# Kernel tuning notes

Measured on AMD Instinct MI355X. Metric: run time of the kernel, lower is better.

## Reference

```python
import jax, jax.numpy as jnp
import numpy as np

VOCAB = 40000
EMB = 128
INNER = 128
Q_LEN = 20


def setup_inputs() -> dict:
    key = jax.random.key(0)
    ks = jax.random.split(key, 16)
    B, S, NB = 32, 512, 20
    std = 0.1
    inp = {
        "memories": jax.random.normal(ks[0], (B, S, NB, EMB), jnp.float32),
        "stories": jax.random.normal(ks[1], (B, S, EMB), jnp.float32),
        "stories_mask": jnp.ones((B, S), jnp.float32),
        "queries": jax.random.randint(ks[2], (B, Q_LEN), 0, VOCAB, jnp.int32),
        "keys": jax.random.randint(ks[3], (NB,), 0, VOCAB, jnp.int32),
        # learned parameters
        "emb_table": jax.random.normal(ks[4], (VOCAB, EMB), jnp.float32) * std,
        "mult_mask": jnp.ones((Q_LEN, EMB), jnp.float32),
        "A": jax.random.normal(ks[5], (EMB, INNER), jnp.float32) * std,
        "Bm": jax.random.normal(ks[6], (EMB, INNER), jnp.float32) * std,
        "C": jax.random.normal(ks[7], (EMB, INNER), jnp.float32) * std,
        "v": jnp.ones((INNER,), jnp.float32),
        "D": jax.random.normal(ks[8], (EMB, INNER), jnp.float32) * std,
        "E": jax.random.normal(ks[9], (EMB, INNER), jnp.float32) * std,
        "F": jax.random.normal(ks[10], (EMB, INNER), jnp.float32) * std,
        "w": jnp.ones((INNER,), jnp.float32),
        "H": jax.random.normal(ks[11], (EMB, EMB), jnp.float32) * std,
        "R": jax.random.normal(ks[12], (EMB, VOCAB), jnp.float32) * std,
    }
    return inp


def reference(memories, stories, stories_mask, queries, keys,
              emb_table, mult_mask, A, Bm, C, v, D, E, F, w, H, R):
    # _reduce_query: embed tokens, apply positional multiplicative mask, sum over positions
    u = jnp.sum(emb_table[queries] * mult_mask, axis=1)            # [B, emb]

    # intratemporal (Bahdanau-style) attention over memory blocks
    ia = jnp.einsum('bsne,ei->bsni', memories, A)                  # [B,S,NB,inner]
    kb = emb_table[keys] @ Bm                                      # [NB,inner]
    qc = u @ C                                                     # [B,inner]
    intr_align = jnp.sum(v * jnp.tanh(ia + kb[None, None] + qc[:, None, None]), axis=3)  # [B,S,NB]
    intr_attn = jax.nn.softmax(intr_align, axis=2)[..., None]      # [B,S,NB,1]
    temporal_memory = jnp.sum(intr_attn * memories, axis=2)        # [B,S,emb]

    # temporal attention over story sentences (with sentence term E, softmax activation)
    td = temporal_memory @ D                                       # [B,S,inner]
    te = stories @ E                                               # [B,S,inner]
    tf = (u @ F)[:, None]                                          # [B,1,inner]
    temporal_align_unmasked = jnp.sum(w * jnp.tanh(td + te + tf), axis=2)  # [B,S]
    temporal_align = temporal_align_unmasked * stories_mask
    # softmax branch: additive -inf mask where stories_mask == 0 (inf*0 NaNs zeroed in torch)
    masked_logits = jnp.where(stories_mask != 0, temporal_align, -jnp.inf)
    temporal_attn = jax.nn.softmax(masked_logits, axis=1)          # [B,S]

    # output readout (standard memory-network head)
    o = jnp.sum(temporal_attn[..., None] * temporal_memory, axis=1)  # [B,emb]
    logits = (o + u @ H) @ R                                         # [B,vocab]
    return logits
```

## Files before the change

### kernel.cpp

```cpp
#include <hip/hip_runtime.h>
#include <hip/hip_bf16.h>

#define B_   32
#define S_   512
#define NB_  20
#define EMB_ 128
#define VOC_ 40000

typedef float f32x4 __attribute__((ext_vector_type(4)));
typedef _Float16 f16x8 __attribute__((ext_vector_type(8)));
typedef __fp16 fp16x2 __attribute__((ext_vector_type(2)));

union FragH { uint4 u; f16x8 h; };
union H2 { fp16x2 h; unsigned u; };

__device__ __forceinline__ unsigned pk2(float a, float b){
  H2 t; t.h = __builtin_amdgcn_cvt_pkrtz(a, b);
  return t.u;
}
__device__ __forceinline__ unsigned short f2h(float x){
  _Float16 h = (_Float16)x;
  return __builtin_bit_cast(unsigned short, h);
}
__device__ __forceinline__ float tanh_fast(float x){
  float xx = fminf(fmaxf(x, -15.f), 15.f);
  float e2 = __builtin_amdgcn_exp2f(xx * 2.8853900817779268f);
  float r  = __builtin_amdgcn_rcpf(e2 + 1.f);
  return fmaf(-2.f, r, 1.f);
}


__global__ __launch_bounds__(128) void prep_kernel(
    const int* __restrict__ queries, const int* __restrict__ keys,
    const float* __restrict__ emb, const float* __restrict__ mmask,
    const float* __restrict__ A, const float* __restrict__ Bm,
    const float* __restrict__ C, const float* __restrict__ D,
    const float* __restrict__ E, const float* __restrict__ F,
    const float* __restrict__ H,
    float* __restrict__ qc_w, float* __restrict__ tf_w,
    float* __restrict__ uh_w, float* __restrict__ kb_w,
    unsigned short* __restrict__ afrag, unsigned short* __restrict__ w2frag)
{
  int bid = blockIdx.x, tid = threadIdx.x;
  if (bid < 32) {
    __shared__ float ulds[128];
    int b = bid;
    float s = 0.f;
    for (int q=0;q<NB_;q++){
      int tok = queries[b*NB_+q];
      s += emb[tok*128+tid]*mmask[q*128+tid];
    }
    ulds[tid] = s;
    __syncthreads();
    float sq=0.f, sf=0.f, sh=0.f;
    for (int e=0;e<128;e++){
      float uv = ulds[e];
      sq += uv*C[e*128+tid];
      sf += uv*F[e*128+tid];
      sh += uv*H[e*128+tid];
    }
    qc_w[b*128+tid]=sq; tf_w[b*128+tid]=sf; uh_w[b*128+tid]=sh;
  } else if (bid < 52) {
    __shared__ float ek[128];
    int n = bid-32;
    int tok = keys[n];
    ek[tid] = emb[tok*128+tid];
    __syncthreads();
    float s=0.f;
    for (int e=0;e<128;e++) s += ek[e]*Bm[e*128+tid];
    kb_w[n*128+tid] = s;
  } else if (bid < 60) {
    int a = bid-52;
    for (int cc=0;cc<2;cc++){
      int c = (a*128+tid)*2+cc;
      int lane = c&63, kc = (c>>6)&3, nt = c>>8;
      int n2 = nt*16 + (lane&15);
      int k0 = kc*32 + (lane>>4)*8;
      alignas(16) unsigned short t[8];
      #pragma unroll
      for (int j=0;j<8;j++) t[j] = f2h(A[(k0+j)*128+n2]);
      *(uint4*)(afrag + c*8) = *(const uint4*)t;
    }
  } else {
    int wb = bid-60;
    for (int cc=0;cc<2;cc++){
      int c = (wb*128+tid)*2+cc;
      int lane = c&63, kc = (c>>6)&7, nt = c>>9;
      int n2 = nt*16 + (lane&15);
      int k0 = kc*32 + (lane>>4)*8;
      alignas(16) unsigned short t[8];
      #pragma unroll
      for (int j=0;j<8;j++){
        int k = k0+j;
        float x = (k<128) ? D[k*128+n2] : E[(k-128)*128+n2];
        t[j] = f2h(x);
      }
      *(uint4*)(w2frag + c*8) = *(const uint4*)t;
    }
  }
}

__global__ __launch_bounds__(256) void k2_kernel(
    const float* __restrict__ mem, const unsigned short* __restrict__ afrag,
    const float* __restrict__ kb_w, const float* __restrict__ qc_w,
    const float* __restrict__ vvec,
    const float* __restrict__ stories, const unsigned short* __restrict__ w2frag,
    const float* __restrict__ tf_w, const float* __restrict__ wvec,
    const float* __restrict__ smask,
    unsigned short* __restrict__ tm_h, float* __restrict__ talign_w)
{
  __shared__ unsigned short mfr[5*4*64*8];
  __shared__ unsigned short a2f[512*8];
  __shared__ float alignP[4*80];
  __shared__ float attns[80];
  __shared__ float partial2[16];

  const int T = 4;
  int tid = threadIdx.x;
  int g0 = blockIdx.x * T;
  int b = g0 >> 7;

  int w = tid>>6, lane = tid&63;
  int lo16 = lane & 15, hi16 = lane >> 4;
  int p2 = tid>>6, e0 = (tid&63)*2;

  int kq = (tid&31)*4;
  int kgs = kq>>5, s2s = (kq>>3)&3, offs = kq&7;
  int r0 = tid>>5;
  int cbs = s2s ^ ((kgs&1)<<2);
  unsigned addr_e = (unsigned)((kgs*64 + ((s2s<<4) | ((r0 ^ cbs) & 15)))*16 + offs*2);
  unsigned addr_o = (unsigned)((kgs*64 + ((s2s<<4) | (((r0^8) ^ cbs) & 15)))*16 + offs*2);

  int i0 = w*32 + lo16, i1 = i0 + 16;
  float qc0 = qc_w[b*128+i0], qc1 = qc_w[b*128+i1];
  float vv0 = vvec[i0],       vv1 = vvec[i1];
  float tf0 = tf_w[b*128+i0], tf1 = tf_w[b*128+i1];
  float wv0 = wvec[i0],       wv1 = wvec[i1];
  const float* kb0 = kb_w + i0;

  float4 pf[10];
  float2 sto, sto_n;

  auto load_tile = [&](int g){
    const float4* gmt = (const float4*)(mem) + (size_t)g*2560 + tid;
    #pragma unroll
    for (int mt=0;mt<5;mt++){
      pf[2*mt]   = gmt[(2*mt)*256];
      pf[2*mt+1] = gmt[(2*mt+1)*256];
    }
  };
  auto store_tile = [&](){
    #pragma unroll
    for (int mt=0;mt<5;mt++){
      *(uint2*)((char*)mfr + addr_e + mt*4096) =
          make_uint2(pk2(pf[2*mt].x,pf[2*mt].y), pk2(pf[2*mt].z,pf[2*mt].w));
      *(uint2*)((char*)mfr + addr_o + mt*4096) =
          make_uint2(pk2(pf[2*mt+1].x,pf[2*mt+1].y), pk2(pf[2*mt+1].z,pf[2*mt+1].w));
    }
  };

  load_tile(g0);
  sto = *(const float2*)(stories + ((size_t)(g0*4+p2))*128 + e0);
  store_tile();
  __syncthreads();

  for (int t=0; t<T; ++t){
    int g = g0 + t;

    f32x4 acc[5][2];
    #pragma unroll
    for (int mt=0;mt<5;mt++){ acc[mt][0]=(f32x4)(0.f); acc[mt][1]=(f32x4)(0.f); }
    #pragma unroll
    for (int kc=0;kc<4;kc++){
      FragH b0, b1;
      b0.u = *(const uint4*)(afrag + ((size_t)((2*w)*4+kc)*64 + lane)*8);
      b1.u = *(const uint4*)(afrag + ((size_t)((2*w+1)*4+kc)*64 + lane)*8);
      int slot = (hi16<<4) | ((lo16 ^ hi16 ^ ((kc&1)<<2)) & 15);
      #pragma unroll
      for (int mt=0;mt<5;mt++){
        FragH a;
        a.u = *(const uint4*)(mfr + ((mt*4+kc)*64 + slot)*8);
        acc[mt][0] = __builtin_amdgcn_mfma_f32_16x16x32_f16(a.h, b0.h, acc[mt][0], 0,0,0);
        acc[mt][1] = __builtin_amdgcn_mfma_f32_16x16x32_f16(a.h, b1.h, acc[mt][1], 0,0,0);
      }
    }
    if (t > 0 && tid < 4){
      float ta = partial2[tid]+partial2[4+tid]+partial2[8+tid]+partial2[12+tid];
      int flat = (g-1)*4+tid;
      float m = smask[flat];
      talign_w[flat] = (m != 0.0f) ? ta*m : -INFINITY;
    }
    #pragma unroll
    for (int mt=0;mt<5;mt++){
      #pragma unroll
      for (int r=0;r<4;r++){
        unsigned row = mt*16 + hi16*4 + r;
        unsigned p = row/20u;
        unsigned n = row - p*20u;
        float z0 = acc[mt][0][r] + kb0[n*128]    + qc0;
        float z1 = acc[mt][1][r] + kb0[n*128+16] + qc1;
        float part = vv0*tanh_fast(z0) + vv1*tanh_fast(z1);
        part += __shfl_xor(part, 1);
        part += __shfl_xor(part, 2);
        part += __shfl_xor(part, 4);
        part += __shfl_xor(part, 8);
        if (lo16 == 0) alignP[w*80+row] = part;
      }
    }
    __syncthreads();

    {
      float av = -1e30f;
      if (lane < 20){
        int idx = w*20 + lane;
        av = alignP[idx] + alignP[80+idx] + alignP[160+idx] + alignP[240+idx];
      }
      float mx = av;
      #pragma unroll
      for (int d=1; d<64; d<<=1) mx = fmaxf(mx, __shfl_xor(mx, d));
      float ev = (lane<20) ? __expf(av - mx) : 0.f;
      float sm = ev;
      #pragma unroll
      for (int d=1; d<64; d<<=1) sm += __shfl_xor(sm, d);
      if (lane<20) attns[w*20+lane] = ev * __builtin_amdgcn_rcpf(sm);
    }
    __syncthreads();

    if (t+1 < T){
      load_tile(g+1);
      sto_n = *(const float2*)(stories + ((size_t)((g+1)*4+p2))*128 + e0);
    }
    unsigned otm;
    {
      int kg = e0>>5, s2 = (e0>>3)&3;
      int cb = s2 ^ ((kg&1)<<2);
      unsigned base = (unsigned)((kg*64 + (s2<<4))*16 + (e0&7)*2);
      float2 o = make_float2(0.f,0.f);
      #define TM_STEP(ROW) { \
        H2 q; q.u = *(const unsigned*)((const char*)mfr + base + (((ROW)>>4)*4096) + ((((ROW)&15) ^ cb) & 15)*16); \
        float a = attns[(ROW)]; \
        o.x += a*(float)q.h[0]; \
        o.y += a*(float)q.h[1]; }
      #define TM_20(P) { \
        TM_STEP((P)*20+0)  TM_STEP((P)*20+1)  TM_STEP((P)*20+2)  TM_STEP((P)*20+3)  \
        TM_STEP((P)*20+4)  TM_STEP((P)*20+5)  TM_STEP((P)*20+6)  TM_STEP((P)*20+7)  \
        TM_STEP((P)*20+8)  TM_STEP((P)*20+9)  TM_STEP((P)*20+10) TM_STEP((P)*20+11) \
        TM_STEP((P)*20+12) TM_STEP((P)*20+13) TM_STEP((P)*20+14) TM_STEP((P)*20+15) \
        TM_STEP((P)*20+16) TM_STEP((P)*20+17) TM_STEP((P)*20+18) TM_STEP((P)*20+19) }
      switch(p2){
        case 0: TM_20(0) break;
        case 1: TM_20(1) break;
        case 2: TM_20(2) break;
        default: TM_20(3) break;
      }
      otm = pk2(o.x, o.y);
      *(unsigned*)(tm_h + ((size_t)g*4+p2)*128 + e0) = otm;
      int kcA = e0>>5;
      int lane2 = (((e0>>3)&3)<<4) | p2;
      *(unsigned*)(a2f + (kcA*64+lane2)*8 + (e0&7)) = otm;
      *(unsigned*)(a2f + ((kcA+4)*64+lane2)*8 + (e0&7)) = pk2(sto.x, sto.y);
    }
    __syncthreads();

    if (t+1 < T){
      store_tile();
      sto = sto_n;
    }
    {
      f32x4 acc0 = (f32x4)(0.f), acc1 = (f32x4)(0.f);
      #pragma unroll
      for (int kc=0;kc<8;kc++){
        FragH af, b0, b1;
        af.u = *(const uint4*)(a2f + (kc*64+lane)*8);
        b0.u = *(const uint4*)(w2frag + ((size_t)((2*w)*8+kc)*64+lane)*8);
        b1.u = *(const uint4*)(w2frag + ((size_t)((2*w+1)*8+kc)*64+lane)*8);
        acc0 = __builtin_amdgcn_mfma_f32_16x16x32_f16(af.h, b0.h, acc0, 0,0,0);
        acc1 = __builtin_amdgcn_mfma_f32_16x16x32_f16(af.h, b1.h, acc1, 0,0,0);
      }
      if (hi16 == 0){
        #pragma unroll
        for (int r=0;r<4;r++){
          float part = wv0*tanh_fast(acc0[r] + tf0) + wv1*tanh_fast(acc1[r] + tf1);
          part += __shfl_xor(part,1);
          part += __shfl_xor(part,2);
          part += __shfl_xor(part,4);
          part += __shfl_xor(part,8);
          if (lo16==0) partial2[w*4+r] = part;
        }
      }
    }
    __syncthreads();
  }
  if (tid < 4){
    float ta = partial2[tid]+partial2[4+tid]+partial2[8+tid]+partial2[12+tid];
    int flat = (g0+T-1)*4+tid;
    float m = smask[flat];
    talign_w[flat] = (m != 0.0f) ? ta*m : -INFINITY;
  }
}

__global__ __launch_bounds__(256) void k3_kernel(
    const float* __restrict__ talign_w, const unsigned short* __restrict__ tm_h,
    const float* __restrict__ uh_w, float* __restrict__ ov_w)
{
  __shared__ float attn[512];
  __shared__ float red[256];
  __shared__ float2 red2[256];
  int bid = blockIdx.x, tid = threadIdx.x;
  int b = bid >> 3, ec = bid & 7;

  float v0 = talign_w[b*512+tid];
  float v1 = talign_w[b*512+256+tid];
  red[tid] = fmaxf(v0,v1);
  __syncthreads();
  for (int s=128;s>0;s>>=1){ if (tid<s) red[tid]=fmaxf(red[tid],red[tid+s]); __syncthreads(); }
  float M = red[0];
  __syncthreads();
  float e0v = __expf(v0-M), e1v = __expf(v1-M);
  red[tid] = e0v+e1v;
  __syncthreads();
  for (int s=128;s>0;s>>=1){ if (tid<s) red[tid]+=red[tid+s]; __syncthreads(); }
  float invZ = 1.f/red[0];
  attn[tid] = e0v*invZ;
  attn[256+tid] = e1v*invZ;
  __syncthreads();

  int e = ec*16 + (tid&7)*2;
  int sg = tid>>3;
  const unsigned short* tmb = tm_h + ((size_t)b*512 + sg*16)*128 + e;
  float2 a2 = make_float2(0.f,0.f);
  #pragma unroll 8
  for (int i=0;i<16;i++){
    H2 q; q.u = *(const unsigned*)(tmb + (size_t)i*128);
    float at = attn[sg*16+i];
    a2.x += at*(float)q.h[0];
    a2.y += at*(float)q.h[1];
  }
  red2[tid] = a2;
  __syncthreads();
  for (int s=128;s>=8;s>>=1){
    if (tid<s){ red2[tid].x += red2[tid+s].x; red2[tid].y += red2[tid+s].y; }
    __syncthreads();
  }
  if (tid<8){
    int e2 = ec*16 + tid*2;
    ov_w[b*128+e2]   = red2[tid].x + uh_w[b*128+e2];
    ov_w[b*128+e2+1] = red2[tid].y + uh_w[b*128+e2+1];
  }
}

__global__ __launch_bounds__(256) void k4_kernel(
    const float* __restrict__ ov_w, const float* __restrict__ R,
    float* __restrict__ out)
{
  int tid = threadIdx.x;
  int j = blockIdx.x*128 + (tid&63)*2;
  if (j >= VOC_) return;
  int bh = tid>>6;
  const float* ovb = ov_w + bh*8*128;
  float2 acc[8];
  #pragma unroll
  for (int bb=0;bb<8;bb++) acc[bb]=make_float2(0.f,0.f);
  for (int e=0;e<128;e+=4){
    float2 r0 = *(const float2*)(&R[(size_t)(e+0)*VOC_ + j]);
    float2 r1 = *(const float2*)(&R[(size_t)(e+1)*VOC_ + j]);
    float2 r2 = *(const float2*)(&R[(size_t)(e+2)*VOC_ + j]);
    float2 r3 = *(const float2*)(&R[(size_t)(e+3)*VOC_ + j]);
    #pragma unroll
    for (int bb=0;bb<8;bb++){
      float4 o = *(const float4*)(&ovb[bb*128+e]);
      acc[bb].x += o.x*r0.x + o.y*r1.x + o.z*r2.x + o.w*r3.x;
      acc[bb].y += o.x*r0.y + o.y*r1.y + o.z*r2.y + o.w*r3.y;
    }
  }
  #pragma unroll
  for (int bb=0;bb<8;bb++)
    *(float2*)(&out[(size_t)(bh*8+bb)*VOC_ + j]) = acc[bb];
}

extern "C" void kernel_launch(void* const* d_in, const int* in_sizes, int n_in,
                              void* d_out, int out_size, void* d_ws, size_t ws_size,
                              hipStream_t stream)
{
  const float* mem    = (const float*)d_in[0];
  const float* stories= (const float*)d_in[1];
  const float* smask  = (const float*)d_in[2];
  const int*   queries= (const int*)d_in[3];
  const int*   keys   = (const int*)d_in[4];
  const float* emb    = (const float*)d_in[5];
  const float* mmask  = (const float*)d_in[6];
  const float* A      = (const float*)d_in[7];
  const float* Bm     = (const float*)d_in[8];
  const float* C      = (const float*)d_in[9];
  const float* vvec   = (const float*)d_in[10];
  const float* D      = (const float*)d_in[11];
  const float* E      = (const float*)d_in[12];
  const float* F      = (const float*)d_in[13];
  const float* wvec   = (const float*)d_in[14];
  const float* H      = (const float*)d_in[15];
  const float* R      = (const float*)d_in[16];
  float* out = (float*)d_out;

  char* ws = (char*)d_ws;
  float* qc_w             = (float*)(ws + 0);
  float* tf_w             = (float*)(ws + 16384);
  float* uh_w             = (float*)(ws + 32768);
  float* kb_w             = (float*)(ws + 49152);
  unsigned short* afrag   = (unsigned short*)(ws + 60416);
  unsigned short* w2frag  = (unsigned short*)(ws + 93184);
  unsigned short* tm_h    = (unsigned short*)(ws + 158720);
  float* talign_w         = (float*)(ws + 4353024);
  float* ov_w             = (float*)(ws + 4418560);

  prep_kernel<<<76,128,0,stream>>>(queries, keys, emb, mmask, A, Bm, C, D, E, F, H,
                                   qc_w, tf_w, uh_w, kb_w, afrag, w2frag);
  k2_kernel<<<1024,256,0,stream>>>(mem, afrag, kb_w, qc_w, vvec,
                                   stories, w2frag, tf_w, wvec, smask,
                                   tm_h, talign_w);
  k3_kernel<<<256,256,0,stream>>>(talign_w, tm_h, uh_w, ov_w);
  k4_kernel<<<313,256,0,stream>>>(ov_w, R, out);
}
```

Measured before the change: 430.3 us.

## Load memory tiles straight into MFMA fragments and drop LDS staging pipeline

The intratemporal attention kernel no longer stages each memory tile through shared memory with a four-tile software pipeline. Each block now handles a single tile: it loads fp32 memory directly from global memory into half-precision MFMA A-fragments, then re-reads the same rows from global memory (expected to hit cache) for the attention-weighted sum. The grid grows fourfold and shared memory use shrinks, which should raise occupancy and remove LDS conversion traffic and barriers. The costs are per-lane strided global loads, a second pass over the memory tile, and no explicit prefetch overlap.

```diff
diff --git a/kernel.cpp b/kernel.cpp
--- a/kernel.cpp
+++ b/kernel.cpp
@@ -28,7 +28,6 @@
   float r  = __builtin_amdgcn_rcpf(e2 + 1.f);
   return fmaf(-2.f, r, 1.f);
 }
-
 
 __global__ __launch_bounds__(128) void prep_kernel(
     const int* __restrict__ queries, const int* __restrict__ keys,
@@ -109,27 +108,19 @@
     const float* __restrict__ smask,
     unsigned short* __restrict__ tm_h, float* __restrict__ talign_w)
 {
-  __shared__ unsigned short mfr[5*4*64*8];
   __shared__ unsigned short a2f[512*8];
   __shared__ float alignP[4*80];
   __shared__ float attns[80];
   __shared__ float partial2[16];
 
-  const int T = 4;
-  int tid = threadIdx.x;
-  int g0 = blockIdx.x * T;
-  int b = g0 >> 7;
+  int g = blockIdx.x, tid = threadIdx.x;
+  int b = g >> 7;
 
   int w = tid>>6, lane = tid&63;
   int lo16 = lane & 15, hi16 = lane >> 4;
-  int p2 = tid>>6, e0 = (tid&63)*2;
-
-  int kq = (tid&31)*4;
-  int kgs = kq>>5, s2s = (kq>>3)&3, offs = kq&7;
-  int r0 = tid>>5;
-  int cbs = s2s ^ ((kgs&1)<<2);
-  unsigned addr_e = (unsigned)((kgs*64 + ((s2s<<4) | ((r0 ^ cbs) & 15)))*16 + offs*2);
-  unsigned addr_o = (unsigned)((kgs*64 + ((s2s<<4) | (((r0^8) ^ cbs) & 15)))*16 + offs*2);
+  int p2 = w, e0 = (tid&63)*2;
+
+  float2 sto = *(const float2*)(stories + ((size_t)(g*4+p2))*128 + e0);
 
   int i0 = w*32 + lo16, i1 = i0 + 16;
   float qc0 = qc_w[b*128+i0], qc1 = qc_w[b*128+i1];
@@ -138,162 +129,111 @@
   float wv0 = wvec[i0],       wv1 = wvec[i1];
   const float* kb0 = kb_w + i0;
 
-  float4 pf[10];
-  float2 sto, sto_n;
-
-  auto load_tile = [&](int g){
-    const float4* gmt = (const float4*)(mem) + (size_t)g*2560 + tid;
+  const float* abase = mem + (size_t)g*10240 + (size_t)lo16*128 + hi16*8;
+  f32x4 acc[5][2];
+  #pragma unroll
+  for (int mt=0;mt<5;mt++){ acc[mt][0]=(f32x4)(0.f); acc[mt][1]=(f32x4)(0.f); }
+  #pragma unroll
+  for (int kc=0;kc<4;kc++){
+    FragH b0, b1;
+    b0.u = *(const uint4*)(afrag + ((size_t)((2*w)*4+kc)*64 + lane)*8);
+    b1.u = *(const uint4*)(afrag + ((size_t)((2*w+1)*4+kc)*64 + lane)*8);
     #pragma unroll
     for (int mt=0;mt<5;mt++){
-      pf[2*mt]   = gmt[(2*mt)*256];
-      pf[2*mt+1] = gmt[(2*mt+1)*256];
-    }
-  };
-  auto store_tile = [&](){
-    #pragma unroll
-    for (int mt=0;mt<5;mt++){
-      *(uint2*)((char*)mfr + addr_e + mt*4096) =
-          make_uint2(pk2(pf[2*mt].x,pf[2*mt].y), pk2(pf[2*mt].z,pf[2*mt].w));
-      *(uint2*)((char*)mfr + addr_o + mt*4096) =
-          make_uint2(pk2(pf[2*mt+1].x,pf[2*mt+1].y), pk2(pf[2*mt+1].z,pf[2*mt+1].w));
-    }
-  };
-
-  load_tile(g0);
-  sto = *(const float2*)(stories + ((size_t)(g0*4+p2))*128 + e0);
-  store_tile();
-  __syncthreads();
-
-  for (int t=0; t<T; ++t){
-    int g = g0 + t;
-
-    f32x4 acc[5][2];
-    #pragma unroll
-    for (int mt=0;mt<5;mt++){ acc[mt][0]=(f32x4)(0.f); acc[mt][1]=(f32x4)(0.f); }
-    #pragma unroll
-    for (int kc=0;kc<4;kc++){
-      FragH b0, b1;
-      b0.u = *(const uint4*)(afrag + ((size_t)((2*w)*4+kc)*64 + lane)*8);
-      b1.u = *(const uint4*)(afrag + ((size_t)((2*w+1)*4+kc)*64 + lane)*8);
-      int slot = (hi16<<4) | ((lo16 ^ hi16 ^ ((kc&1)<<2)) & 15);
-      #pragma unroll
-      for (int mt=0;mt<5;mt++){
-        FragH a;
-        a.u = *(const uint4*)(mfr + ((mt*4+kc)*64 + slot)*8);
-        acc[mt][0] = __builtin_amdgcn_mfma_f32_16x16x32_f16(a.h, b0.h, acc[mt][0], 0,0,0);
-        acc[mt][1] = __builtin_amdgcn_mfma_f32_16x16x32_f16(a.h, b1.h, acc[mt][1], 0,0,0);
-      }
-    }
-    if (t > 0 && tid < 4){
-      float ta = partial2[tid]+partial2[4+tid]+partial2[8+tid]+partial2[12+tid];
-      int flat = (g-1)*4+tid;
-      float m = smask[flat];
-      talign_w[flat] = (m != 0.0f) ? ta*m : -INFINITY;
-    }
-    #pragma unroll
-    for (int mt=0;mt<5;mt++){
+      const float* src = abase + kc*32 + mt*2048;
+      float4 f0 = *(const float4*)(src);
+      float4 f1 = *(const float4*)(src+4);
+      FragH a;
+      a.u = make_uint4(pk2(f0.x,f0.y), pk2(f0.z,f0.w),
+                       pk2(f1.x,f1.y), pk2(f1.z,f1.w));
+      acc[mt][0] = __builtin_amdgcn_mfma_f32_16x16x32_f16(a.h, b0.h, acc[mt][0], 0,0,0);
+      acc[mt][1] = __builtin_amdgcn_mfma_f32_16x16x32_f16(a.h, b1.h, acc[mt][1], 0,0,0);
+    }
+  }
+
+  #pragma unroll
+  for (int mt=0;mt<5;mt++){
+    #pragma unroll
+    for (int r=0;r<4;r++){
+      unsigned row = mt*16 + hi16*4 + r;
+      unsigned p = row/20u;
+      unsigned n = row - p*20u;
+      float z0 = acc[mt][0][r] + kb0[n*128]    + qc0;
+      float z1 = acc[mt][1][r] + kb0[n*128+16] + qc1;
+      float part = vv0*tanh_fast(z0) + vv1*tanh_fast(z1);
+      part += __shfl_xor(part, 1);
+      part += __shfl_xor(part, 2);
+      part += __shfl_xor(part, 4);
+      part += __shfl_xor(part, 8);
+      if (lo16 == 0) alignP[w*80+row] = part;
+    }
+  }
+  __syncthreads();
+
+  {
+    float av = -1e30f;
+    if (lane < 20){
+      int idx = w*20 + lane;
+      av = alignP[idx] + alignP[80+idx] + alignP[160+idx] + alignP[240+idx];
+    }
+    float mx = av;
+    #pragma unroll
+    for (int d=1; d<64; d<<=1) mx = fmaxf(mx, __shfl_xor(mx, d));
+    float ev = (lane<20) ? __expf(av - mx) : 0.f;
+    float sm = ev;
+    #pragma unroll
+    for (int d=1; d<64; d<<=1) sm += __shfl_xor(sm, d);
+    if (lane<20) attns[w*20+lane] = ev * __builtin_amdgcn_rcpf(sm);
+  }
+
+  unsigned otm;
+  {
+    const float* tmem = mem + (size_t)g*10240 + (size_t)p2*20*128 + e0;
+    float2 o = make_float2(0.f,0.f);
+    #pragma unroll
+    for (int n=0;n<NB_;n++){
+      float2 f = *(const float2*)(tmem + n*128);
+      float a = attns[p2*20+n];
+      o.x += a*f.x;
+      o.y += a*f.y;
+    }
+    otm = pk2(o.x, o.y);
+    *(unsigned*)(tm_h + ((size_t)g*4+p2)*128 + e0) = otm;
+    int kcA = e0>>5;
+    int lane2 = (((e0>>3)&3)<<4) | p2;
+    *(unsigned*)(a2f + (kcA*64+lane2)*8 + (e0&7)) = otm;
+    *(unsigned*)(a2f + ((kcA+4)*64+lane2)*8 + (e0&7)) = pk2(sto.x, sto.y);
+  }
+  __syncthreads();
+
+  {
+    f32x4 acc0 = (f32x4)(0.f), acc1 = (f32x4)(0.f);
+    #pragma unroll
+    for (int kc=0;kc<8;kc++){
+      FragH af, b0, b1;
+      af.u = *(const uint4*)(a2f + (kc*64+lane)*8);
+      b0.u = *(const uint4*)(w2frag + ((size_t)((2*w)*8+kc)*64+lane)*8);
+      b1.u = *(const uint4*)(w2frag + ((size_t)((2*w+1)*8+kc)*64+lane)*8);
+      acc0 = __builtin_amdgcn_mfma_f32_16x16x32_f16(af.h, b0.h, acc0, 0,0,0);
+      acc1 = __builtin_amdgcn_mfma_f32_16x16x32_f16(af.h, b1.h, acc1, 0,0,0);
+    }
+    if (hi16 == 0){
       #pragma unroll
       for (int r=0;r<4;r++){
-        unsigned row = mt*16 + hi16*4 + r;
-        unsigned p = row/20u;
-        unsigned n = row - p*20u;
-        float z0 = acc[mt][0][r] + kb0[n*128]    + qc0;
-        float z1 = acc[mt][1][r] + kb0[n*128+16] + qc1;
-        float part = vv0*tanh_fast(z0) + vv1*tanh_fast(z1);
-        part += __shfl_xor(part, 1);
-        part += __shfl_xor(part, 2);
-        part += __shfl_xor(part, 4);
-        part += __shfl_xor(part, 8);
-        if (lo16 == 0) alignP[w*80+row] = part;
+        float part = wv0*tanh_fast(acc0[r] + tf0) + wv1*tanh_fast(acc1[r] + tf1);
+        part += __shfl_xor(part,1);
+        part += __shfl_xor(part,2);
+        part += __shfl_xor(part,4);
+        part += __shfl_xor(part,8);
+        if (lo16==0) partial2[w*4+r] = part;
       }
     }
-    __syncthreads();
-
-    {
-      float av = -1e30f;
-      if (lane < 20){
-        int idx = w*20 + lane;
-        av = alignP[idx] + alignP[80+idx] + alignP[160+idx] + alignP[240+idx];
-      }
-      float mx = av;
-      #pragma unroll
-      for (int d=1; d<64; d<<=1) mx = fmaxf(mx, __shfl_xor(mx, d));
-      float ev = (lane<20) ? __expf(av - mx) : 0.f;
-      float sm = ev;
-      #pragma unroll
-      for (int d=1; d<64; d<<=1) sm += __shfl_xor(sm, d);
-      if (lane<20) attns[w*20+lane] = ev * __builtin_amdgcn_rcpf(sm);
-    }
-    __syncthreads();
-
-    if (t+1 < T){
-      load_tile(g+1);
-      sto_n = *(const float2*)(stories + ((size_t)((g+1)*4+p2))*128 + e0);
-    }
-    unsigned otm;
-    {
-      int kg = e0>>5, s2 = (e0>>3)&3;
-      int cb = s2 ^ ((kg&1)<<2);
-      unsigned base = (unsigned)((kg*64 + (s2<<4))*16 + (e0&7)*2);
-      float2 o = make_float2(0.f,0.f);
-      #define TM_STEP(ROW) { \
-        H2 q; q.u = *(const unsigned*)((const char*)mfr + base + (((ROW)>>4)*4096) + ((((ROW)&15) ^ cb) & 15)*16); \
-        float a = attns[(ROW)]; \
-        o.x += a*(float)q.h[0]; \
-        o.y += a*(float)q.h[1]; }
-      #define TM_20(P) { \
-        TM_STEP((P)*20+0)  TM_STEP((P)*20+1)  TM_STEP((P)*20+2)  TM_STEP((P)*20+3)  \
-        TM_STEP((P)*20+4)  TM_STEP((P)*20+5)  TM_STEP((P)*20+6)  TM_STEP((P)*20+7)  \
-        TM_STEP((P)*20+8)  TM_STEP((P)*20+9)  TM_STEP((P)*20+10) TM_STEP((P)*20+11) \
-        TM_STEP((P)*20+12) TM_STEP((P)*20+13) TM_STEP((P)*20+14) TM_STEP((P)*20+15) \
-        TM_STEP((P)*20+16) TM_STEP((P)*20+17) TM_STEP((P)*20+18) TM_STEP((P)*20+19) }
-      switch(p2){
-        case 0: TM_20(0) break;
-        case 1: TM_20(1) break;
-        case 2: TM_20(2) break;
-        default: TM_20(3) break;
-      }
-      otm = pk2(o.x, o.y);
-      *(unsigned*)(tm_h + ((size_t)g*4+p2)*128 + e0) = otm;
-      int kcA = e0>>5;
-      int lane2 = (((e0>>3)&3)<<4) | p2;
-      *(unsigned*)(a2f + (kcA*64+lane2)*8 + (e0&7)) = otm;
-      *(unsigned*)(a2f + ((kcA+4)*64+lane2)*8 + (e0&7)) = pk2(sto.x, sto.y);
-    }
-    __syncthreads();
-
-    if (t+1 < T){
-      store_tile();
-      sto = sto_n;
-    }
-    {
-      f32x4 acc0 = (f32x4)(0.f), acc1 = (f32x4)(0.f);
-      #pragma unroll
-      for (int kc=0;kc<8;kc++){
-        FragH af, b0, b1;
-        af.u = *(const uint4*)(a2f + (kc*64+lane)*8);
-        b0.u = *(const uint4*)(w2frag + ((size_t)((2*w)*8+kc)*64+lane)*8);
-        b1.u = *(const uint4*)(w2frag + ((size_t)((2*w+1)*8+kc)*64+lane)*8);
-        acc0 = __builtin_amdgcn_mfma_f32_16x16x32_f16(af.h, b0.h, acc0, 0,0,0);
-        acc1 = __builtin_amdgcn_mfma_f32_16x16x32_f16(af.h, b1.h, acc1, 0,0,0);
-      }
-      if (hi16 == 0){
-        #pragma unroll
-        for (int r=0;r<4;r++){
-          float part = wv0*tanh_fast(acc0[r] + tf0) + wv1*tanh_fast(acc1[r] + tf1);
-          part += __shfl_xor(part,1);
-          part += __shfl_xor(part,2);
-          part += __shfl_xor(part,4);
-          part += __shfl_xor(part,8);
-          if (lo16==0) partial2[w*4+r] = part;
-        }
-      }
-    }
-    __syncthreads();
-  }
+  }
+  __syncthreads();
+
   if (tid < 4){
     float ta = partial2[tid]+partial2[4+tid]+partial2[8+tid]+partial2[12+tid];
-    int flat = (g0+T-1)*4+tid;
+    int flat = g*4+tid;
     float m = smask[flat];
     talign_w[flat] = (m != 0.0f) ? ta*m : -INFINITY;
   }
@@ -414,7 +354,7 @@
 
   prep_kernel<<<76,128,0,stream>>>(queries, keys, emb, mmask, A, Bm, C, D, E, F, H,
                                    qc_w, tf_w, uh_w, kb_w, afrag, w2frag);
-  k2_kernel<<<1024,256,0,stream>>>(mem, afrag, kb_w, qc_w, vvec,
+  k2_kernel<<<4096,256,0,stream>>>(mem, afrag, kb_w, qc_w, vvec,
                                    stories, w2frag, tf_w, wvec, smask,
                                    tm_h, talign_w);
   k3_kernel<<<256,256,0,stream>>>(talign_w, tm_h, uh_w, ov_w);
```

After: 423.6 us. No clear change (-1.6%).
